# Performance work log

Hardware: AMD Instinct MI355X
Metric: run time of the kernel (lower is better)

Reference implementation:

```python
import jax, jax.numpy as jnp
import numpy as np

N_NODES = 50000
N_EDGES = 800000
IN_FEATS = 256
OUT_FEATS = 128


def setup_inputs() -> dict:
    key = jax.random.key(0)
    k1, k2, k3, k4 = jax.random.split(key, 4)
    feat = jax.random.normal(k1, (N_NODES, IN_FEATS), dtype=jnp.float32)
    # xavier uniform init for weight [in, out]
    limit = float(np.sqrt(6.0 / (IN_FEATS + OUT_FEATS)))
    weight = jax.random.uniform(k2, (IN_FEATS, OUT_FEATS), minval=-limit, maxval=limit, dtype=jnp.float32)
    bias = jnp.zeros((OUT_FEATS,), dtype=jnp.float32)
    src = jax.random.randint(k3, (N_EDGES,), 0, N_NODES, dtype=jnp.int32)
    dst = jax.random.randint(k4, (N_EDGES,), 0, N_NODES, dtype=jnp.int32)
    return {"feat": feat, "weight": weight, "bias": bias, "src": src, "dst": dst}


def reference(feat, weight, bias, src, dst):
    N = feat.shape[0]
    in_f, out_f = weight.shape
    # right normalization: 1 / out_degree(src node), clamped to >= 1
    deg = jax.ops.segment_sum(jnp.ones(src.shape[0], dtype=feat.dtype), src, num_segments=N)
    norm = (1.0 / jnp.maximum(deg, 1.0))[:, None]  # [N,1]
    if in_f > out_f:
        # transform first (cheaper messages), then normalize + aggregate
        h = jnp.matmul(feat, weight) * norm          # [N, out]
        rst = jax.ops.segment_sum(h[src], dst, num_segments=N)  # scatter-sum over edges
    else:
        h = feat * norm                               # [N, in]
        rst = jax.ops.segment_sum(h[src], dst, num_segments=N)
        rst = jnp.matmul(rst, weight)
    return rst + bias
```

## Files before the change

### kernel.cpp

```cpp
#include <hip/hip_runtime.h>

#define N_NODES 50000
#define N_EDGES 800000
#define IN_F 256
#define OUT_F 128

#define CHUNKS 128
#define EPC (N_EDGES / CHUNKS)
#define BINW (N_NODES / 4)
#define NWORDS (N_NODES / 4)
#define RGB 196
#define HIST_BLOCKS (2 * CHUNKS)
#define CPW (CHUNKS / 4)

typedef __attribute__((ext_vector_type(8))) short short8;
typedef __attribute__((ext_vector_type(4))) float float4_t;

__device__ __forceinline__ short f2bf(float f) {
  unsigned u = __builtin_bit_cast(unsigned, f);
  u = u + 0x7FFFu + ((u >> 16) & 1u);
  return (short)(u >> 16);
}

__device__ __forceinline__ float bflo(unsigned u) {
  return __builtin_bit_cast(float, u << 16);
}
__device__ __forceinline__ float bfhi(unsigned u) {
  return __builtin_bit_cast(float, u & 0xFFFF0000u);
}

__global__ __launch_bounds__(256) void hist_kernel(const int* __restrict__ src,
                                                   const int* __restrict__ dst,
                                                   unsigned char* __restrict__ pdst8,
                                                   unsigned char* __restrict__ psrc8,
                                                   unsigned char* __restrict__ rank8,
                                                   const float* __restrict__ W,
                                                   short* __restrict__ Wf,
                                                   int* __restrict__ cursor) {
  __shared__ unsigned bins[BINW];
  int b = blockIdx.x;
  int t = threadIdx.x;
  if (b >= HIST_BLOCKS) {
    int bb = b - HIST_BLOCKS;
    if (bb == 0 && t == 0) *cursor = 0;
#pragma unroll
    for (int i = 0; i < 64; ++i) {
      int idx = bb * 16384 + i * 256 + t;
      int k = idx >> 7, n = idx & 127;
      int s = k >> 5, q = (k >> 3) & 3, j = k & 7;
      int tt = n >> 4, m = n & 15;
      Wf[(((s * 8 + tt) * 16 + m) * 32) + q * 8 + j] = f2bf(W[idx]);
    }
    return;
  }
  int h = b >> 7;
  int c = b & 127;
  for (int j = t; j < BINW; j += 256) bins[j] = 0;
  __syncthreads();
  const int* key = h ? src : dst;
  int e0 = c * EPC;

  auto process = [&](int v, int eI) {
    unsigned sh = (v & 3) * 8;
    unsigned old = atomicAdd(&bins[v >> 2], 1u << sh);
    if (!h) rank8[eI] = (unsigned char)((old >> sh) & 0xFFu);
  };

#pragma unroll 2
  for (int tile = 0; tile < 6; ++tile) {
    int i = tile * 1024 + t;
    int k0 = key[e0 + i];
    int k1 = key[e0 + i + 256];
    int k2 = key[e0 + i + 512];
    int k3 = key[e0 + i + 768];
    process(k0, e0 + i);
    process(k1, e0 + i + 256);
    process(k2, e0 + i + 512);
    process(k3, e0 + i + 768);
  }
  {
    int i = 6144 + t;
    if (i < EPC) process(key[e0 + i], e0 + i);
  }
  __syncthreads();
  unsigned* p32 = (unsigned*)((h ? psrc8 : pdst8) + (size_t)c * N_NODES);
  for (int j = t; j < BINW; j += 256) p32[j] = bins[j];
}

__global__ __launch_bounds__(256) void reduceoff_kernel(const unsigned char* __restrict__ pdst8,
                                                        const unsigned char* __restrict__ psrc8,
                                                        unsigned char* __restrict__ delta8,
                                                        int* __restrict__ cnt,
                                                        int* __restrict__ row_start,
                                                        int* __restrict__ cursor,
                                                        float* __restrict__ norm) {
  __shared__ unsigned tot[4][64];
  int g = blockIdx.x, side = blockIdx.y;
  int t = threadIdx.x;
  int w = t >> 6, l = t & 63;
  int wd = g * 64 + l;
  bool ok = wd < NWORDS;
  int wdc = ok ? wd : NWORDS - 1;
  const unsigned* P = (const unsigned*)(side == 0 ? pdst8 : psrc8);

  unsigned vals[CPW];
  unsigned s = 0;
#pragma unroll
  for (int i = 0; i < CPW; ++i) {
    vals[i] = P[(size_t)(w * CPW + i) * NWORDS + wdc];
    s += vals[i];
  }
  tot[w][l] = s;
  __syncthreads();

  if (side == 0) {
    unsigned base = 0;
#pragma unroll
    for (int w2 = 0; w2 < 4; ++w2)
      if (w2 < w) base += tot[w2][l];
    unsigned run = base;
    unsigned* D = (unsigned*)delta8;
    if (ok) {
#pragma unroll
      for (int i = 0; i < CPW; ++i) {
        D[(size_t)(w * CPW + i) * NWORDS + wd] = run;
        run += vals[i];
      }
    }
    if (w == 0) {
      unsigned ftot = tot[0][l] + tot[1][l] + tot[2][l] + tot[3][l];
      if (!ok) ftot = 0;
      int c0 = ftot & 255, c1 = (ftot >> 8) & 255, c2 = (ftot >> 16) & 255, c3 = ftot >> 24;
      int T = c0 + c1 + c2 + c3;
      int x = T;
#pragma unroll
      for (int off = 1; off < 64; off <<= 1) {
        int y = __shfl_up(x, off);
        if (l >= off) x += y;
      }
      int waveTotal = __shfl(x, 63);
      int sb = 0;
      if (l == 63) sb = atomicAdd(cursor, waveTotal);
      sb = __shfl(sb, 63);
      int E = sb + x - T;
      if (ok) {
        int4 cv = {c0, c1, c2, c3};
        int4 rv = {E, E + c0, E + c0 + c1, E + c0 + c1 + c2};
        ((int4*)cnt)[wd] = cv;
        ((int4*)row_start)[wd] = rv;
      }
    }
  } else {
    if (w == 0 && ok) {
      unsigned ftot = tot[0][l] + tot[1][l] + tot[2][l] + tot[3][l];
      float4 nv;
      int d0 = ftot & 255, d1 = (ftot >> 8) & 255, d2 = (ftot >> 16) & 255, d3 = (int)(ftot >> 24);
      nv.x = 1.0f / (float)(d0 > 1 ? d0 : 1);
      nv.y = 1.0f / (float)(d1 > 1 ? d1 : 1);
      nv.z = 1.0f / (float)(d2 > 1 ? d2 : 1);
      nv.w = 1.0f / (float)(d3 > 1 ? d3 : 1);
      ((float4*)norm)[wd] = nv;
    }
  }
}

__global__ __launch_bounds__(256) void scatter_kernel(const int* __restrict__ src,
                                                      const int* __restrict__ dst,
                                                      const int* __restrict__ row_start,
                                                      const unsigned char* __restrict__ delta8,
                                                      const unsigned char* __restrict__ rank8,
                                                      int* __restrict__ eidx) {
  int tid = blockIdx.x * 256 + threadIdx.x;
  int e = tid * 4;
  if (e >= N_EDGES) return;
  int4 d4 = *(const int4*)(dst + e);
  int4 s4 = *(const int4*)(src + e);
  unsigned rr = *(const unsigned*)(rank8 + e);
  int dd[4] = {d4.x, d4.y, d4.z, d4.w};
  int ss[4] = {s4.x, s4.y, s4.z, s4.w};
#pragma unroll
  for (int k = 0; k < 4; ++k) {
    int c = (e + k) / EPC;
    int d = dd[k];
    int pos = row_start[d] + (int)delta8[(size_t)c * N_NODES + d] + (int)((rr >> (8 * k)) & 0xFFu);
    eidx[pos] = ss[k];
  }
}

__global__ __launch_bounds__(128) void gemm_kernel(const float* __restrict__ feat,
                                                   const short* __restrict__ Wf,
                                                   const float* __restrict__ norm,
                                                   unsigned short* __restrict__ h) {
  int tid = threadIdx.x;
  int w = tid >> 6, l = tid & 63;
  int m = l & 15, q = l >> 4;
  long base = (long)blockIdx.x * 64 + w * 32;

  float4_t acc[2][8];
#pragma unroll
  for (int r = 0; r < 2; ++r)
#pragma unroll
    for (int t = 0; t < 8; ++t) acc[r][t] = (float4_t)(0.0f);

  long row0 = base + m;
  long row1 = base + 16 + m;
  long r0c = row0 < N_NODES - 1 ? row0 : N_NODES - 1;
  long r1c = row1 < N_NODES - 1 ? row1 : N_NODES - 1;
  const float* a0p = feat + (size_t)r0c * IN_F;
  const float* a1p = feat + (size_t)r1c * IN_F;
  const short8* bb = (const short8*)Wf;

#pragma unroll
  for (int s = 0; s < 8; ++s) {
    int k0 = s * 32 + q * 8;
    float4_t av0a = *(const float4_t*)(a0p + k0);
    float4_t av0b = *(const float4_t*)(a0p + k0 + 4);
    float4_t av1a = *(const float4_t*)(a1p + k0);
    float4_t av1b = *(const float4_t*)(a1p + k0 + 4);
    short8 fa0, fa1;
#pragma unroll
    for (int i = 0; i < 4; ++i) {
      fa0[i] = f2bf(av0a[i]);
      fa0[i + 4] = f2bf(av0b[i]);
      fa1[i] = f2bf(av1a[i]);
      fa1[i + 4] = f2bf(av1b[i]);
    }
#pragma unroll
    for (int t = 0; t < 8; ++t) {
      short8 fb = bb[((s * 8 + t) * 16 + m) * 4 + q];
      acc[0][t] = __builtin_amdgcn_mfma_f32_16x16x32_bf16(fa0, fb, acc[0][t], 0, 0, 0);
      acc[1][t] = __builtin_amdgcn_mfma_f32_16x16x32_bf16(fa1, fb, acc[1][t], 0, 0, 0);
    }
  }

#pragma unroll
  for (int r = 0; r < 2; ++r) {
#pragma unroll
    for (int i = 0; i < 4; ++i) {
      long row = base + r * 16 + q * 4 + i;
      if (row < N_NODES) {
        float nm = norm[row];
        size_t ho = (size_t)row * OUT_F;
#pragma unroll
        for (int t = 0; t < 8; ++t) {
          h[ho + t * 16 + m] = (unsigned short)f2bf(acc[r][t][i] * nm);
        }
      }
    }
  }
}

__global__ __launch_bounds__(256) void agg_kernel(const unsigned short* __restrict__ h,
                                                  const int* __restrict__ row_start,
                                                  const int* __restrict__ cnt,
                                                  const int* __restrict__ eidx,
                                                  const float* __restrict__ bias,
                                                  float* __restrict__ out) {
  int w = threadIdx.x >> 6, l = threadIdx.x & 63;
  int d = blockIdx.x * 4 + w;
  int rs = row_start[d], re = rs + cnt[d];
  const unsigned* __restrict__ hu = (const unsigned*)h;
  int rowsel = l >> 5, cp = l & 31;
  float a0 = 0.f, a1 = 0.f, a2 = 0.f, a3 = 0.f;
  for (int bse = rs; bse < re; bse += 64) {
    int n = re - bse; if (n > 64) n = 64;
    int e = (l < n) ? eidx[bse + l] : 0;
    int half = (n + 1) >> 1;
    int j = 0;
    for (; j + 2 <= half; j += 2) {
      int i0 = 2 * j + rowsel;
      int i1 = i0 + 2;
      int s0 = __shfl(e, i0);
      int s1 = __shfl(e, i1);
      uint2 v0 = *(const uint2*)(hu + (size_t)s0 * 64 + 2 * cp);
      uint2 v1 = *(const uint2*)(hu + (size_t)s1 * 64 + 2 * cp);
      if (i0 >= n) { v0.x = 0; v0.y = 0; }
      if (i1 >= n) { v1.x = 0; v1.y = 0; }
      a0 += bflo(v0.x); a1 += bfhi(v0.x); a2 += bflo(v0.y); a3 += bfhi(v0.y);
      a0 += bflo(v1.x); a1 += bfhi(v1.x); a2 += bflo(v1.y); a3 += bfhi(v1.y);
    }
    for (; j < half; ++j) {
      int i0 = 2 * j + rowsel;
      int s0 = __shfl(e, i0);
      uint2 v0 = *(const uint2*)(hu + (size_t)s0 * 64 + 2 * cp);
      if (i0 >= n) { v0.x = 0; v0.y = 0; }
      a0 += bflo(v0.x); a1 += bfhi(v0.x); a2 += bflo(v0.y); a3 += bfhi(v0.y);
    }
  }
  a0 += __shfl_xor(a0, 32);
  a1 += __shfl_xor(a1, 32);
  a2 += __shfl_xor(a2, 32);
  a3 += __shfl_xor(a3, 32);
  if (rowsel == 0) {
    float4 bv = ((const float4*)bias)[cp];
    float4 o;
    o.x = a0 + bv.x; o.y = a1 + bv.y; o.z = a2 + bv.z; o.w = a3 + bv.w;
    ((float4*)(out + (size_t)d * OUT_F))[cp] = o;
  }
}

extern "C" void kernel_launch(void* const* d_in, const int* in_sizes, int n_in,
                              void* d_out, int out_size, void* d_ws, size_t ws_size,
                              hipStream_t stream) {
  const float* feat = (const float*)d_in[0];
  const float* weight = (const float*)d_in[1];
  const float* bias = (const float*)d_in[2];
  const int* src = (const int*)d_in[3];
  const int* dst = (const int*)d_in[4];
  float* out = (float*)d_out;

  char* ws = (char*)d_ws;
  size_t off = 0;
  auto alloc = [&](size_t bytes) -> void* {
    void* p = ws + off;
    off += (bytes + 511) & ~(size_t)511;
    return p;
  };
  int* cursor = (int*)alloc(4);
  int* cnt = (int*)alloc(N_NODES * 4);
  int* row_start = (int*)alloc(N_NODES * 4);
  float* norm = (float*)alloc(N_NODES * 4);
  int* eidx = (int*)alloc(N_EDGES * 4);
  short* Wf = (short*)alloc(IN_F * OUT_F * 2);
  unsigned short* h = (unsigned short*)alloc((size_t)N_NODES * OUT_F * 2);
  unsigned char* pdst8 = (unsigned char*)alloc((size_t)CHUNKS * N_NODES);
  unsigned char* psrc8 = (unsigned char*)alloc((size_t)CHUNKS * N_NODES);
  unsigned char* delta8 = (unsigned char*)alloc((size_t)CHUNKS * N_NODES);
  unsigned char* rank8 = (unsigned char*)alloc((size_t)N_EDGES);
  (void)off; (void)ws_size; (void)in_sizes; (void)n_in; (void)out_size;

  hipLaunchKernelGGL(hist_kernel, dim3(HIST_BLOCKS + 2), dim3(256), 0, stream,
                     src, dst, pdst8, psrc8, rank8, weight, Wf, cursor);
  hipLaunchKernelGGL(reduceoff_kernel, dim3(RGB, 2), dim3(256), 0, stream,
                     pdst8, psrc8, delta8, cnt, row_start, cursor, norm);
  hipLaunchKernelGGL(scatter_kernel, dim3((N_EDGES / 4 + 255) / 256), dim3(256), 0, stream,
                     src, dst, row_start, delta8, rank8, eidx);
  hipLaunchKernelGGL(gemm_kernel, dim3((N_NODES + 63) / 64), dim3(128), 0, stream, feat, Wf, norm, h);
  hipLaunchKernelGGL(agg_kernel, dim3(N_NODES / 4), dim3(256), 0, stream, h, row_start, cnt, eidx, bias, out);
}
```

Measured before the change: 186.5 us.

## Fuse scatter and GEMM into one launch, widen histogram copies, unroll aggregation

Merges the edge-scatter kernel and the bf16 MFMA GEMM kernel into a single launch: the first blocks run the GEMM (now 4 waves, 128 rows per block) and the rest run the scatter, so the two independent stages overlap. This removes one launch and the idle tail between them. The histogram kernel now zeroes and copies its LDS bins with 128-bit accesses. The aggregation loop gains a 4-way unrolled gather path to keep more loads in flight. The cost is higher register pressure in the combined kernel, which may lower occupancy for the scatter blocks.

```diff
diff --git a/kernel.cpp b/kernel.cpp
--- a/kernel.cpp
+++ b/kernel.cpp
@@ -12,6 +12,9 @@
 #define RGB 196
 #define HIST_BLOCKS (2 * CHUNKS)
 #define CPW (CHUNKS / 4)
+
+#define GEMM_BLOCKS 391
+#define SCAT_BLOCKS 782
 
 typedef __attribute__((ext_vector_type(8))) short short8;
 typedef __attribute__((ext_vector_type(4))) float float4_t;
@@ -55,7 +58,8 @@
   }
   int h = b >> 7;
   int c = b & 127;
-  for (int j = t; j < BINW; j += 256) bins[j] = 0;
+  uint4* b4 = (uint4*)bins;
+  for (int j = t; j < BINW / 4; j += 256) b4[j] = (uint4){0u, 0u, 0u, 0u};
   __syncthreads();
   const int* key = h ? src : dst;
   int e0 = c * EPC;
@@ -83,8 +87,9 @@
     if (i < EPC) process(key[e0 + i], e0 + i);
   }
   __syncthreads();
-  unsigned* p32 = (unsigned*)((h ? psrc8 : pdst8) + (size_t)c * N_NODES);
-  for (int j = t; j < BINW; j += 256) p32[j] = bins[j];
+  uint4* p128 = (uint4*)((h ? psrc8 : pdst8) + (size_t)c * N_NODES);
+  const uint4* s128 = (const uint4*)bins;
+  for (int j = t; j < BINW / 4; j += 256) p128[j] = s128[j];
 }
 
 __global__ __launch_bounds__(256) void reduceoff_kernel(const unsigned char* __restrict__ pdst8,
@@ -164,88 +169,90 @@
   }
 }
 
-__global__ __launch_bounds__(256) void scatter_kernel(const int* __restrict__ src,
-                                                      const int* __restrict__ dst,
-                                                      const int* __restrict__ row_start,
-                                                      const unsigned char* __restrict__ delta8,
-                                                      const unsigned char* __restrict__ rank8,
-                                                      int* __restrict__ eidx) {
-  int tid = blockIdx.x * 256 + threadIdx.x;
-  int e = tid * 4;
-  if (e >= N_EDGES) return;
-  int4 d4 = *(const int4*)(dst + e);
-  int4 s4 = *(const int4*)(src + e);
-  unsigned rr = *(const unsigned*)(rank8 + e);
-  int dd[4] = {d4.x, d4.y, d4.z, d4.w};
-  int ss[4] = {s4.x, s4.y, s4.z, s4.w};
-#pragma unroll
-  for (int k = 0; k < 4; ++k) {
-    int c = (e + k) / EPC;
-    int d = dd[k];
-    int pos = row_start[d] + (int)delta8[(size_t)c * N_NODES + d] + (int)((rr >> (8 * k)) & 0xFFu);
-    eidx[pos] = ss[k];
-  }
-}
-
-__global__ __launch_bounds__(128) void gemm_kernel(const float* __restrict__ feat,
-                                                   const short* __restrict__ Wf,
-                                                   const float* __restrict__ norm,
-                                                   unsigned short* __restrict__ h) {
+__global__ __launch_bounds__(256) void sg_kernel(const float* __restrict__ feat,
+                                                 const short* __restrict__ Wf,
+                                                 const float* __restrict__ norm,
+                                                 unsigned short* __restrict__ h,
+                                                 const int* __restrict__ src,
+                                                 const int* __restrict__ dst,
+                                                 const int* __restrict__ row_start,
+                                                 const unsigned char* __restrict__ delta8,
+                                                 const unsigned char* __restrict__ rank8,
+                                                 int* __restrict__ eidx) {
+  int b = blockIdx.x;
   int tid = threadIdx.x;
-  int w = tid >> 6, l = tid & 63;
-  int m = l & 15, q = l >> 4;
-  long base = (long)blockIdx.x * 64 + w * 32;
-
-  float4_t acc[2][8];
-#pragma unroll
-  for (int r = 0; r < 2; ++r)
-#pragma unroll
-    for (int t = 0; t < 8; ++t) acc[r][t] = (float4_t)(0.0f);
-
-  long row0 = base + m;
-  long row1 = base + 16 + m;
-  long r0c = row0 < N_NODES - 1 ? row0 : N_NODES - 1;
-  long r1c = row1 < N_NODES - 1 ? row1 : N_NODES - 1;
-  const float* a0p = feat + (size_t)r0c * IN_F;
-  const float* a1p = feat + (size_t)r1c * IN_F;
-  const short8* bb = (const short8*)Wf;
-
-#pragma unroll
-  for (int s = 0; s < 8; ++s) {
-    int k0 = s * 32 + q * 8;
-    float4_t av0a = *(const float4_t*)(a0p + k0);
-    float4_t av0b = *(const float4_t*)(a0p + k0 + 4);
-    float4_t av1a = *(const float4_t*)(a1p + k0);
-    float4_t av1b = *(const float4_t*)(a1p + k0 + 4);
-    short8 fa0, fa1;
-#pragma unroll
-    for (int i = 0; i < 4; ++i) {
-      fa0[i] = f2bf(av0a[i]);
-      fa0[i + 4] = f2bf(av0b[i]);
-      fa1[i] = f2bf(av1a[i]);
-      fa1[i + 4] = f2bf(av1b[i]);
-    }
-#pragma unroll
-    for (int t = 0; t < 8; ++t) {
-      short8 fb = bb[((s * 8 + t) * 16 + m) * 4 + q];
-      acc[0][t] = __builtin_amdgcn_mfma_f32_16x16x32_bf16(fa0, fb, acc[0][t], 0, 0, 0);
-      acc[1][t] = __builtin_amdgcn_mfma_f32_16x16x32_bf16(fa1, fb, acc[1][t], 0, 0, 0);
-    }
-  }
-
-#pragma unroll
-  for (int r = 0; r < 2; ++r) {
-#pragma unroll
-    for (int i = 0; i < 4; ++i) {
-      long row = base + r * 16 + q * 4 + i;
-      if (row < N_NODES) {
-        float nm = norm[row];
-        size_t ho = (size_t)row * OUT_F;
-#pragma unroll
-        for (int t = 0; t < 8; ++t) {
-          h[ho + t * 16 + m] = (unsigned short)f2bf(acc[r][t][i] * nm);
+  if (b < GEMM_BLOCKS) {
+    int w = tid >> 6, l = tid & 63;
+    int m = l & 15, q = l >> 4;
+    long base = (long)b * 128 + w * 32;
+
+    float4_t acc[2][8];
+#pragma unroll
+    for (int r = 0; r < 2; ++r)
+#pragma unroll
+      for (int t = 0; t < 8; ++t) acc[r][t] = (float4_t)(0.0f);
+
+    long row0 = base + m;
+    long row1 = base + 16 + m;
+    long r0c = row0 < N_NODES - 1 ? row0 : N_NODES - 1;
+    long r1c = row1 < N_NODES - 1 ? row1 : N_NODES - 1;
+    const float* a0p = feat + (size_t)r0c * IN_F;
+    const float* a1p = feat + (size_t)r1c * IN_F;
+    const short8* bb = (const short8*)Wf;
+
+#pragma unroll
+    for (int s = 0; s < 8; ++s) {
+      int k0 = s * 32 + q * 8;
+      float4_t av0a = *(const float4_t*)(a0p + k0);
+      float4_t av0b = *(const float4_t*)(a0p + k0 + 4);
+      float4_t av1a = *(const float4_t*)(a1p + k0);
+      float4_t av1b = *(const float4_t*)(a1p + k0 + 4);
+      short8 fa0, fa1;
+#pragma unroll
+      for (int i = 0; i < 4; ++i) {
+        fa0[i] = f2bf(av0a[i]);
+        fa0[i + 4] = f2bf(av0b[i]);
+        fa1[i] = f2bf(av1a[i]);
+        fa1[i + 4] = f2bf(av1b[i]);
+      }
+#pragma unroll
+      for (int t = 0; t < 8; ++t) {
+        short8 fb = bb[((s * 8 + t) * 16 + m) * 4 + q];
+        acc[0][t] = __builtin_amdgcn_mfma_f32_16x16x32_bf16(fa0, fb, acc[0][t], 0, 0, 0);
+        acc[1][t] = __builtin_amdgcn_mfma_f32_16x16x32_bf16(fa1, fb, acc[1][t], 0, 0, 0);
+      }
+    }
+
+#pragma unroll
+    for (int r = 0; r < 2; ++r) {
+#pragma unroll
+      for (int i = 0; i < 4; ++i) {
+        long row = base + r * 16 + q * 4 + i;
+        if (row < N_NODES) {
+          float nm = norm[row];
+          size_t ho = (size_t)row * OUT_F;
+#pragma unroll
+          for (int t = 0; t < 8; ++t) {
+            h[ho + t * 16 + m] = (unsigned short)f2bf(acc[r][t][i] * nm);
+          }
         }
       }
+    }
+  } else {
+    int gt = (b - GEMM_BLOCKS) * 256 + tid;
+    int e = gt * 4;
+    if (e >= N_EDGES) return;
+    int4 d4 = *(const int4*)(dst + e);
+    int4 s4 = *(const int4*)(src + e);
+    unsigned rr = *(const unsigned*)(rank8 + e);
+    int dd[4] = {d4.x, d4.y, d4.z, d4.w};
+    int ss[4] = {s4.x, s4.y, s4.z, s4.w};
+#pragma unroll
+    for (int k = 0; k < 4; ++k) {
+      int c = (e + k) / EPC;
+      int d = dd[k];
+      int pos = row_start[d] + (int)delta8[(size_t)c * N_NODES + d] + (int)((rr >> (8 * k)) & 0xFFu);
+      eidx[pos] = ss[k];
     }
   }
 }
@@ -267,6 +274,25 @@
     int e = (l < n) ? eidx[bse + l] : 0;
     int half = (n + 1) >> 1;
     int j = 0;
+    for (; j + 4 <= half; j += 4) {
+      int i0 = 2 * j + rowsel;
+      int s0 = __shfl(e, i0);
+      int s1 = __shfl(e, i0 + 2);
+      int s2 = __shfl(e, i0 + 4);
+      int s3 = __shfl(e, i0 + 6);
+      uint2 v0 = *(const uint2*)(hu + (size_t)s0 * 64 + 2 * cp);
+      uint2 v1 = *(const uint2*)(hu + (size_t)s1 * 64 + 2 * cp);
+      uint2 v2 = *(const uint2*)(hu + (size_t)s2 * 64 + 2 * cp);
+      uint2 v3 = *(const uint2*)(hu + (size_t)s3 * 64 + 2 * cp);
+      if (i0 >= n) { v0.x = 0; v0.y = 0; }
+      if (i0 + 2 >= n) { v1.x = 0; v1.y = 0; }
+      if (i0 + 4 >= n) { v2.x = 0; v2.y = 0; }
+      if (i0 + 6 >= n) { v3.x = 0; v3.y = 0; }
+      a0 += bflo(v0.x); a1 += bfhi(v0.x); a2 += bflo(v0.y); a3 += bfhi(v0.y);
+      a0 += bflo(v1.x); a1 += bfhi(v1.x); a2 += bflo(v1.y); a3 += bfhi(v1.y);
+      a0 += bflo(v2.x); a1 += bfhi(v2.x); a2 += bflo(v2.y); a3 += bfhi(v2.y);
+      a0 += bflo(v3.x); a1 += bfhi(v3.x); a2 += bflo(v3.y); a3 += bfhi(v3.y);
+    }
     for (; j + 2 <= half; j += 2) {
       int i0 = 2 * j + rowsel;
       int i1 = i0 + 2;
@@ -333,8 +359,7 @@
                      src, dst, pdst8, psrc8, rank8, weight, Wf, cursor);
   hipLaunchKernelGGL(reduceoff_kernel, dim3(RGB, 2), dim3(256), 0, stream,
                      pdst8, psrc8, delta8, cnt, row_start, cursor, norm);
-  hipLaunchKernelGGL(scatter_kernel, dim3((N_EDGES / 4 + 255) / 256), dim3(256), 0, stream,
-                     src, dst, row_start, delta8, rank8, eidx);
-  hipLaunchKernelGGL(gemm_kernel, dim3((N_NODES + 63) / 64), dim3(128), 0, stream, feat, Wf, norm, h);
+  hipLaunchKernelGGL(sg_kernel, dim3(GEMM_BLOCKS + SCAT_BLOCKS), dim3(256), 0, stream,
+                     feat, Wf, norm, h, src, dst, row_start, delta8, rank8, eidx);
   hipLaunchKernelGGL(agg_kernel, dim3(N_NODES / 4), dim3(256), 0, stream, h, row_start, cnt, eidx, bias, out);
 }
```

Result: no change. 185.1 us (-0.7%).
